# Kernel optimization log

Measured on AMD Instinct MI355X. Metric: run time of the kernel, lower is better.

## Reference

```python
import jax, jax.numpy as jnp
import numpy as np

MAX_LENGTH = 128
SOS_TOKEN = 0

V, H, B, S = 16384, 512, 32, 128


def gru_cell(x, h, Wih, Whh, bih, bhh):
    # torch nn.GRU gate layout: [r, z, n]
    gi = x @ Wih.T + bih  # [B, 3H]
    gh = h @ Whh.T + bhh  # [B, 3H]
    ir, iz, inn = jnp.split(gi, 3, axis=-1)
    hr, hz, hn = jnp.split(gh, 3, axis=-1)
    r = jax.nn.sigmoid(ir + hr)
    z = jax.nn.sigmoid(iz + hz)
    n = jnp.tanh(inn + r * hn)
    return (1.0 - z) * n + z * h


def setup_inputs() -> dict:
    key = jax.random.key(0)
    ks = jax.random.split(key, 13)
    w = lambda k, shape: (jax.random.normal(k, shape, dtype=jnp.float32) * 0.1)
    return {
        "input_tensor": jax.random.randint(ks[0], (B, S), 0, V),
        "enc_emb": w(ks[1], (V, H)),
        "enc_Wih": w(ks[2], (3 * H, H)),
        "enc_Whh": w(ks[3], (3 * H, H)),
        "enc_bih": w(ks[4], (3 * H,)),
        "enc_bhh": w(ks[5], (3 * H,)),
        "dec_emb": w(ks[6], (V, H)),
        "dec_Wih": w(ks[7], (3 * H, H)),
        "dec_Whh": w(ks[8], (3 * H, H)),
        "dec_bih": w(ks[9], (3 * H,)),
        "dec_bhh": w(ks[10], (3 * H,)),
        "out_W": w(ks[11], (V, H)),
        "out_b": w(ks[12], (V,)),
    }


def reference(input_tensor, enc_emb, enc_Wih, enc_Whh, enc_bih, enc_bhh,
              dec_emb, dec_Wih, dec_Whh, dec_bih, dec_bhh, out_W, out_b):
    batch = input_tensor.shape[0]

    # ---- encoder: embedding + GRU over source sequence ----
    xs = enc_emb[input_tensor]                 # [B, S, H]
    xs = jnp.swapaxes(xs, 0, 1)                # [S, B, H]

    def enc_step(h, x):
        h = gru_cell(x, h, enc_Wih, enc_Whh, enc_bih, enc_bhh)
        return h, h

    h0 = jnp.zeros((batch, H), dtype=xs.dtype)
    enc_hidden, enc_outputs = jax.lax.scan(enc_step, h0, xs)
    # enc_outputs: [S, B, H] (unused downstream, as in the original)

    # ---- decoder: free-run (target_tensor=None) with argmax feedback ----
    sos = jnp.full((batch,), SOS_TOKEN, dtype=jnp.int32)

    def dec_step(carry, _):
        h, tok = carry
        x = dec_emb[tok]                       # [B, H]
        h = gru_cell(x, h, dec_Wih, dec_Whh, dec_bih, dec_bhh)
        logits = h @ out_W.T + out_b           # [B, V]
        tok = jnp.argmax(logits, axis=-1).astype(jnp.int32)  # topk(1) feedback
        return (h, tok), logits

    (dec_hidden, _), logits = jax.lax.scan(dec_step, (enc_hidden, sos), None,
                                           length=MAX_LENGTH)
    logits = jnp.swapaxes(logits, 0, 1)        # [B, MAX_LENGTH, V]
    log_probs = jax.nn.log_softmax(logits, axis=-1)
    return log_probs, dec_hidden
```

## Files before the change

kernel.cpp:

```cpp
#include <hip/hip_runtime.h>

#define HDIM 512
#define BATCH 32
#define SEQ 128
#define VOCAB 16384
#define NBLK 256
#define NGRU 128
#define NTHR 256
#define SLOTP 32
#define HLDS_W 516

typedef unsigned long long u64;
typedef unsigned int u32;

static __device__ __forceinline__ u64 aload64(const u64* p) {
    return __hip_atomic_load(p, __ATOMIC_RELAXED, __HIP_MEMORY_SCOPE_AGENT);
}
static __device__ __forceinline__ void astore64(u64* p, u64 v) {
    __hip_atomic_store(p, v, __ATOMIC_RELAXED, __HIP_MEMORY_SCOPE_AGENT);
}
static __device__ __forceinline__ u32 aload32(const u32* p) {
    return __hip_atomic_load(p, __ATOMIC_RELAXED, __HIP_MEMORY_SCOPE_AGENT);
}
static __device__ __forceinline__ void astore32(u32* p, u32 v) {
    __hip_atomic_store(p, v, __ATOMIC_RELAXED, __HIP_MEMORY_SCOPE_AGENT);
}
static __device__ __forceinline__ void astore32f(float* p, float v) {
    __hip_atomic_store((u32*)p, __float_as_uint(v), __ATOMIC_RELAXED,
                       __HIP_MEMORY_SCOPE_AGENT);
}

static __device__ __forceinline__ float4 ld4(const float* p) {
    return *reinterpret_cast<const float4*>(p);
}
static __device__ __forceinline__ float dot4(float4 a, float4 b) {
    return a.x*b.x + a.y*b.y + a.z*b.z + a.w*b.w;
}
static __device__ __forceinline__ u32 ford(float f) {
    u32 b = __float_as_uint(f);
    return b ^ ((b >> 31) ? 0xFFFFFFFFu : 0x80000000u);
}
static __device__ __forceinline__ u64 shfl_xor_u64(u64 x, int m) {
    int lo = __shfl_xor((int)(u32)x, m);
    int hi = __shfl_xor((int)(u32)(x >> 32), m);
    return ((u64)(u32)hi << 32) | (u32)lo;
}

static __device__ __forceinline__ void pollN(const u32* slots, u32 target,
                                             int tid, int per) {
    if (tid < 64) {
        int it = 0;
        for (;;) {
            bool ok = true;
            #pragma unroll
            for (int k = 0; k < 4; ++k)
                if (k < per)
                    ok &= (aload32(&slots[(tid * per + k) * SLOTP]) >= target);
            if (__ballot(ok) == ~0ull) break;
            if (it > 64)      __builtin_amdgcn_s_sleep(16);
            else if (it > 8)  __builtin_amdgcn_s_sleep(2);
            ++it;
        }
    }
    __syncthreads();
    asm volatile("" ::: "memory");
}

static __device__ __forceinline__ void stage_wide(float* hlf, const float* hsrc, int tid) {
    #pragma unroll
    for (int g = 0; g < 2; ++g) {
        float4 v[8];
        #pragma unroll
        for (int k = 0; k < 8; ++k) {
            int q = (g * 8 + k) * NTHR + tid;
            asm volatile("global_load_dwordx4 %0, %1, off sc1"
                         : "=v"(v[k]) : "v"(hsrc + q * 4));
        }
        asm volatile("s_waitcnt vmcnt(0)" ::: "memory");
        __builtin_amdgcn_sched_barrier(0);
        #pragma unroll
        for (int k = 0; k < 8; ++k) {
            int q = (g * 8 + k) * NTHR + tid;
            int w = q * 4;
            *reinterpret_cast<float4*>(hlf + (w >> 9) * HLDS_W + (w & 511)) = v[k];
        }
    }
}

static __device__ __forceinline__ void stage_h(float* hlf, const float* hglob, int tid) {
    const u64* src = (const u64*)hglob;
    #pragma unroll
    for (int it = 0; it < 32; ++it) {
        int q = it * NTHR + tid;
        int w = q * 2;
        u64 v = aload64(src + q);
        *reinterpret_cast<u64*>(hlf + (w >> 9) * HLDS_W + (w & 511)) = v;
    }
}

static __device__ __forceinline__ void gru_core(
    int blk, int tid, const int* toks, const float* hlf, float* hout,
    const float* __restrict__ Wih, const float* __restrict__ Whh,
    const float* __restrict__ bih, const float* __restrict__ bhh,
    const float* __restrict__ emb)
{
    const int wave = tid >> 6;
    const int lane = tid & 63;
    const int kh   = lane >> 5;
    const int b    = lane & 31;
    const int j    = blk * 4 + wave;

    const int tok = toks[b];
    const float* xrow = emb + (size_t)tok * HDIM + kh * 256;
    const float* hrow = hlf + b * HLDS_W + kh * 256;
    const float* wir = Wih + (size_t)(0*HDIM + j) * HDIM + kh * 256;
    const float* wiz = Wih + (size_t)(1*HDIM + j) * HDIM + kh * 256;
    const float* win = Wih + (size_t)(2*HDIM + j) * HDIM + kh * 256;
    const float* whr = Whh + (size_t)(0*HDIM + j) * HDIM + kh * 256;
    const float* whz = Whh + (size_t)(1*HDIM + j) * HDIM + kh * 256;
    const float* whn = Whh + (size_t)(2*HDIM + j) * HDIM + kh * 256;

    float pr = 0.f, pz = 0.f, pxn = 0.f, phn = 0.f;
    #pragma unroll 4
    for (int k4 = 0; k4 < 64; ++k4) {
        float4 x4 = ld4(xrow + k4*4);
        float4 h4 = ld4(hrow + k4*4);
        pr  += dot4(x4, ld4(wir + k4*4)) + dot4(h4, ld4(whr + k4*4));
        pz  += dot4(x4, ld4(wiz + k4*4)) + dot4(h4, ld4(whz + k4*4));
        pxn += dot4(x4, ld4(win + k4*4));
        phn += dot4(h4, ld4(whn + k4*4));
    }
    pr  += __shfl_xor(pr, 32);
    pz  += __shfl_xor(pz, 32);
    pxn += __shfl_xor(pxn, 32);
    phn += __shfl_xor(phn, 32);

    if (kh == 0) {
        float r = 1.f / (1.f + expf(-(pr + bih[j]      + bhh[j])));
        float z = 1.f / (1.f + expf(-(pz + bih[HDIM+j] + bhh[HDIM+j])));
        float n = tanhf(pxn + bih[2*HDIM+j] + r * (phn + bhh[2*HDIM+j]));
        float hprev = hlf[b * HLDS_W + j];
        astore32f(hout + b * HDIM + j, (1.f - z) * n + z * hprev);
    }
}

static __device__ __forceinline__ void logits_core(
    int blk, int tid, const float* hlf,
    const float* __restrict__ outW, const float* __restrict__ outb,
    float* __restrict__ out, int t, u64* pk)
{
    const int vloc = tid & 63;
    const int bq   = tid >> 6;
    const int v    = blk * 64 + vloc;
    const float* wrow = outW + (size_t)v * HDIM;

    float acc[4][8];
    #pragma unroll
    for (int q = 0; q < 4; ++q)
        #pragma unroll
        for (int i = 0; i < 8; ++i) acc[q][i] = 0.f;

    #pragma unroll
    for (int q = 0; q < 4; ++q) {
        for (int k4 = 0; k4 < 32; ++k4) {
            float4 w4 = ld4(wrow + q*128 + k4*4);
            #pragma unroll
            for (int i = 0; i < 8; ++i) {
                float4 h4 = ld4(hlf + (bq*8 + i) * HLDS_W + q*128 + k4*4);
                acc[q][i] += dot4(w4, h4);
            }
        }
    }
    const float vbias = outb[v];
    #pragma unroll
    for (int i = 0; i < 8; ++i) {
        const int b = bq*8 + i;
        float s = ((acc[0][i] + acc[1][i]) + acc[2][i]) + acc[3][i] + vbias;
        __builtin_nontemporal_store(s, &out[(size_t)b*(SEQ*VOCAB) + (size_t)t*VOCAB + v]);
        u64 key = ((u64)ford(s) << 32) | (u32)(~(u32)v);
        #pragma unroll
        for (int d = 1; d < 64; d <<= 1) {
            u64 o = shfl_xor_u64(key, d);
            if (o > key) key = o;
        }
        if (vloc == 0) astore64(pk + b * NBLK + blk, key);
    }
}

static __device__ __forceinline__ void argmax_finalize(
    int tid, const u64* pk, u64 (*redk)[8], int* tok_s)
{
    const int fb = tid >> 3, kc = tid & 7;
    const u64* p = pk + fb * NBLK;
    u64 best = aload64(p + kc);
    #pragma unroll 4
    for (int k = 1; k < 32; ++k) {
        u64 x = aload64(p + kc + k * 8);
        if (x > best) best = x;
    }
    redk[fb][kc] = best;
    __syncthreads();
    if (tid < BATCH) {
        u64 bb = redk[tid][0];
        #pragma unroll
        for (int c = 1; c < 8; ++c) { u64 x = redk[tid][c]; if (x > bb) bb = x; }
        tok_s[tid] = (int)(~(u32)bb);
    }
}

static __device__ __forceinline__ void softmax_row(float* p, int tid,
                                                   float* redm, float* reds) {
    float4 vals[16];
    float m = -3.4e38f;
    #pragma unroll
    for (int i = 0; i < 16; ++i) {
        vals[i] = ld4(p + (i * 256 + tid) * 4);
        m = fmaxf(m, fmaxf(fmaxf(vals[i].x, vals[i].y), fmaxf(vals[i].z, vals[i].w)));
    }
    #pragma unroll
    for (int d = 1; d < 64; d <<= 1) m = fmaxf(m, __shfl_xor(m, d));
    if ((tid & 63) == 0) redm[tid >> 6] = m;
    __syncthreads();
    m = fmaxf(fmaxf(redm[0], redm[1]), fmaxf(redm[2], redm[3]));
    float s = 0.f;
    #pragma unroll
    for (int i = 0; i < 16; ++i) {
        s += expf(vals[i].x - m) + expf(vals[i].y - m)
           + expf(vals[i].z - m) + expf(vals[i].w - m);
    }
    #pragma unroll
    for (int d = 1; d < 64; d <<= 1) s += __shfl_xor(s, d);
    if ((tid & 63) == 0) reds[tid >> 6] = s;
    __syncthreads();
    s = reds[0] + reds[1] + reds[2] + reds[3];
    const float lg = m + logf(s);
    #pragma unroll
    for (int i = 0; i < 16; ++i) {
        float4 r;
        r.x = vals[i].x - lg; r.y = vals[i].y - lg;
        r.z = vals[i].z - lg; r.w = vals[i].w - lg;
        *reinterpret_cast<float4*>(p + (i * 256 + tid) * 4) = r;
    }
    __syncthreads();
}

__global__ __launch_bounds__(NTHR, 1) void seq2seq_main(
    const int* __restrict__ input,
    const float* __restrict__ enc_emb, const float* __restrict__ enc_Wih,
    const float* __restrict__ enc_Whh, const float* __restrict__ enc_bih,
    const float* __restrict__ enc_bhh,
    const float* __restrict__ dec_emb, const float* __restrict__ dec_Wih,
    const float* __restrict__ dec_Whh, const float* __restrict__ dec_bih,
    const float* __restrict__ dec_bhh,
    const float* __restrict__ out_W, const float* __restrict__ out_b,
    float* __restrict__ out, float* hglob, u64* pk,
    u32* hslot, u32* pkslot)
{
    __shared__ __align__(16) float hl[BATCH][HLDS_W];
    __shared__ int tok_s[BATCH];
    __shared__ u64 redk[BATCH][8];

    const int tid = threadIdx.x;
    const int blk = blockIdx.x;
    float* hlf = &hl[0][0];

    for (int i = tid; i < BATCH * HLDS_W; i += NTHR) hlf[i] = 0.f;
    __syncthreads();

    if (blk < NGRU) {
        for (int t = 0; t < SEQ; ++t) {
            float* hgo = hglob + ((t + 1) & 1) * (BATCH * HDIM);
            if (tid < BATCH) tok_s[tid] = input[tid * SEQ + t];
            __syncthreads();
            gru_core(blk, tid, tok_s, hlf, hgo,
                     enc_Wih, enc_Whh, enc_bih, enc_bhh, enc_emb);
            __syncthreads();
            if (tid == 0) astore32(&hslot[blk * SLOTP], (u32)(t + 1));
            pollN(hslot, (u32)(t + 1), tid, 2);
            stage_wide(hlf, hgo, tid);
            __syncthreads();
        }
    }

    for (int t = 0; t < SEQ; ++t) {
        float* hgo = hglob + ((t + 1) & 1) * (BATCH * HDIM);

        if (blk < NGRU) {
            if (t == 0) {
                if (tid < BATCH) tok_s[tid] = 0;
                __syncthreads();
            } else {
                pollN(pkslot, (u32)t, tid, 4);
                argmax_finalize(tid, pk, redk, tok_s);
                __syncthreads();
            }
            gru_core(blk, tid, tok_s, hlf, hgo,
                     dec_Wih, dec_Whh, dec_bih, dec_bhh, dec_emb);
            __syncthreads();
            if (tid == 0) astore32(&hslot[blk * SLOTP], (u32)(SEQ + t + 1));
        }

        pollN(hslot, (u32)(SEQ + t + 1), tid, 2);
        stage_wide(hlf, hgo, tid);
        __syncthreads();
        logits_core(blk, tid, hlf, out_W, out_b, out, t, pk);
        __syncthreads();
        if (tid == 0) astore32(&pkslot[blk * SLOTP], (u32)(t + 1));
    }

    if (blk < 16) {
        const int idx = blk * 1024 + tid * 4;
        const int b = idx >> 9, j = idx & 511;
        *reinterpret_cast<float4*>(out + (size_t)BATCH * SEQ * VOCAB + idx) =
            *reinterpret_cast<const float4*>(&hl[b][j]);
    }
}

#define SLOT_U32 ((128 + 256) * SLOTP)
__global__ __launch_bounds__(256) void init_kernel(float* __restrict__ h0,
                                                   u32* __restrict__ slots) {
    int i = blockIdx.x * 256 + threadIdx.x;
    if (i < BATCH * HDIM) h0[i] = 0.f;
    if (i < SLOT_U32) slots[i] = 0;
}

__global__ __launch_bounds__(256) void gru_step_fb(
    const float* __restrict__ h_in, float* __restrict__ h_out,
    const float* __restrict__ Wih, const float* __restrict__ Whh,
    const float* __restrict__ bih, const float* __restrict__ bhh,
    const float* __restrict__ emb,
    const int* __restrict__ enc_tokens, int t, const u64* __restrict__ pk)
{
    __shared__ __align__(16) float hlt[BATCH][HLDS_W];
    __shared__ int tok_s[BATCH];
    __shared__ u64 redk[BATCH][8];
    const int tid = threadIdx.x;

    if (enc_tokens != nullptr) {
        if (tid < BATCH) tok_s[tid] = enc_tokens[tid * SEQ + t];
    } else if (t == 0) {
        if (tid < BATCH) tok_s[tid] = 0;
    } else {
        argmax_finalize(tid, pk, redk, tok_s);
    }
    stage_h(&hlt[0][0], h_in, tid);
    __syncthreads();
    gru_core(blockIdx.x, tid, tok_s, &hlt[0][0], h_out, Wih, Whh, bih, bhh, emb);
}

__global__ __launch_bounds__(256) void logits_fb(
    const float* __restrict__ h, const float* __restrict__ outW,
    const float* __restrict__ outb, float* __restrict__ out,
    int t, u64* __restrict__ pk)
{
    __shared__ __align__(16) float hlt[BATCH][HLDS_W];
    const int tid = threadIdx.x;
    stage_h(&hlt[0][0], h, tid);
    __syncthreads();
    logits_core(blockIdx.x, tid, &hlt[0][0], outW, outb, out, t, pk);
}

__global__ __launch_bounds__(256) void copy_fb(const float* __restrict__ src,
                                               float* __restrict__ dst, int n) {
    int i = blockIdx.x * 256 + threadIdx.x;
    if (i < n) dst[i] = src[i];
}

__global__ __launch_bounds__(256) void softmax_kernel(float* __restrict__ out) {
    __shared__ float redm[4];
    __shared__ float reds[4];
    softmax_row(out + (size_t)blockIdx.x * VOCAB, threadIdx.x, redm, reds);
}

extern "C" void kernel_launch(void* const* d_in, const int* in_sizes, int n_in,
                              void* d_out, int out_size, void* d_ws, size_t ws_size,
                              hipStream_t stream) {
    const int*   input    = (const int*)  d_in[0];
    const float* enc_emb  = (const float*)d_in[1];
    const float* enc_Wih  = (const float*)d_in[2];
    const float* enc_Whh  = (const float*)d_in[3];
    const float* enc_bih  = (const float*)d_in[4];
    const float* enc_bhh  = (const float*)d_in[5];
    const float* dec_emb  = (const float*)d_in[6];
    const float* dec_Wih  = (const float*)d_in[7];
    const float* dec_Whh  = (const float*)d_in[8];
    const float* dec_bih  = (const float*)d_in[9];
    const float* dec_bhh  = (const float*)d_in[10];
    const float* out_W    = (const float*)d_in[11];
    const float* out_b    = (const float*)d_in[12];

    float* out = (float*)d_out;
    char*  ws  = (char*)d_ws;

    float* hglob  = (float*)ws;
    u64*   pk     = (u64*)(ws + 131072);
    u32*   hslot  = (u32*)(ws + 196608);
    u32*   pkslot = (u32*)(ws + 212992);

    init_kernel<<<dim3(64), dim3(256), 0, stream>>>(hglob, hslot);

    void* args[] = {
        (void*)&input, (void*)&enc_emb, (void*)&enc_Wih, (void*)&enc_Whh,
        (void*)&enc_bih, (void*)&enc_bhh,
        (void*)&dec_emb, (void*)&dec_Wih, (void*)&dec_Whh, (void*)&dec_bih,
        (void*)&dec_bhh, (void*)&out_W, (void*)&out_b,
        (void*)&out, (void*)&hglob, (void*)&pk,
        (void*)&hslot, (void*)&pkslot
    };
    hipError_t rc = hipLaunchCooperativeKernel((void*)seq2seq_main,
                                               dim3(NBLK), dim3(NTHR),
                                               args, 0, stream);
    if (rc != hipSuccess) {
        float* hb[2] = { hglob, hglob + BATCH * HDIM };
        for (int t = 0; t < SEQ; ++t) {
            gru_step_fb<<<dim3(NGRU), dim3(256), 0, stream>>>(
                hb[t & 1], hb[(t + 1) & 1],
                enc_Wih, enc_Whh, enc_bih, enc_bhh, enc_emb, input, t, nullptr);
        }
        for (int t = 0; t < SEQ; ++t) {
            gru_step_fb<<<dim3(NGRU), dim3(256), 0, stream>>>(
                hb[t & 1], hb[(t + 1) & 1],
                dec_Wih, dec_Whh, dec_bih, dec_bhh, dec_emb, nullptr, t, pk);
            logits_fb<<<dim3(NBLK), dim3(256), 0, stream>>>(
                hb[(t + 1) & 1], out_W, out_b, out, t, pk);
        }
        copy_fb<<<dim3((BATCH * HDIM + 255) / 256), dim3(256), 0, stream>>>(
            hglob, out + (size_t)BATCH * SEQ * VOCAB, BATCH * HDIM);
    }

    softmax_kernel<<<dim3(BATCH * SEQ), dim3(256), 0, stream>>>(out);
}
```

Baseline: 9.805 ms.

## Use 1024-thread blocks, fewer GRU blocks, and K-split logits with LDS reduction

Raises the persistent cooperative kernel to 1024 threads per block. GRU rows are now spread over 32 blocks (16 rows each) instead of 128, so fewer blocks take part in each hidden-state barrier poll. The logits GEMV splits the K dimension across four wave groups and reduces partial sums through a new shared-memory buffer before the argmax step. This cuts per-step synchronisation fan-in and adds parallelism to the logits work, at the cost of more LDS, an extra block barrier, and possibly lower occupancy or higher register pressure.

```diff
diff --git a/kernel.cpp b/kernel.cpp
--- a/kernel.cpp
+++ b/kernel.cpp
@@ -5,8 +5,8 @@
 #define SEQ 128
 #define VOCAB 16384
 #define NBLK 256
-#define NGRU 128
-#define NTHR 256
+#define NTHR 1024
+#define NGRU 32
 #define SLOTP 32
 #define HLDS_W 516
 
@@ -47,15 +47,17 @@
 }
 
 static __device__ __forceinline__ void pollN(const u32* slots, u32 target,
-                                             int tid, int per) {
+                                             int tid, int nslots) {
     if (tid < 64) {
+        const int per = (nslots + 63) >> 6;
         int it = 0;
         for (;;) {
             bool ok = true;
-            #pragma unroll
-            for (int k = 0; k < 4; ++k)
-                if (k < per)
-                    ok &= (aload32(&slots[(tid * per + k) * SLOTP]) >= target);
+            for (int k = 0; k < per; ++k) {
+                int idx = tid * per + k;
+                if (idx < nslots)
+                    ok &= (aload32(&slots[idx * SLOTP]) >= target);
+            }
             if (__ballot(ok) == ~0ull) break;
             if (it > 64)      __builtin_amdgcn_s_sleep(16);
             else if (it > 8)  __builtin_amdgcn_s_sleep(2);
@@ -67,23 +69,20 @@
 }
 
 static __device__ __forceinline__ void stage_wide(float* hlf, const float* hsrc, int tid) {
-    #pragma unroll
-    for (int g = 0; g < 2; ++g) {
-        float4 v[8];
-        #pragma unroll
-        for (int k = 0; k < 8; ++k) {
-            int q = (g * 8 + k) * NTHR + tid;
-            asm volatile("global_load_dwordx4 %0, %1, off sc1"
-                         : "=v"(v[k]) : "v"(hsrc + q * 4));
-        }
-        asm volatile("s_waitcnt vmcnt(0)" ::: "memory");
-        __builtin_amdgcn_sched_barrier(0);
-        #pragma unroll
-        for (int k = 0; k < 8; ++k) {
-            int q = (g * 8 + k) * NTHR + tid;
-            int w = q * 4;
-            *reinterpret_cast<float4*>(hlf + (w >> 9) * HLDS_W + (w & 511)) = v[k];
-        }
+    float4 v[4];
+    #pragma unroll
+    for (int k = 0; k < 4; ++k) {
+        int q = k * NTHR + tid;
+        asm volatile("global_load_dwordx4 %0, %1, off sc1"
+                     : "=v"(v[k]) : "v"(hsrc + q * 4));
+    }
+    asm volatile("s_waitcnt vmcnt(0)" ::: "memory");
+    __builtin_amdgcn_sched_barrier(0);
+    #pragma unroll
+    for (int k = 0; k < 4; ++k) {
+        int q = k * NTHR + tid;
+        int w = q * 4;
+        *reinterpret_cast<float4*>(hlf + (w >> 9) * HLDS_W + (w & 511)) = v[k];
     }
 }
 
@@ -91,24 +90,22 @@
     const u64* src = (const u64*)hglob;
     #pragma unroll
     for (int it = 0; it < 32; ++it) {
-        int q = it * NTHR + tid;
+        int q = it * 256 + tid;
         int w = q * 2;
         u64 v = aload64(src + q);
         *reinterpret_cast<u64*>(hlf + (w >> 9) * HLDS_W + (w & 511)) = v;
     }
 }
 
-static __device__ __forceinline__ void gru_core(
-    int blk, int tid, const int* toks, const float* hlf, float* hout,
+static __device__ __forceinline__ void gru_j(
+    int j, int tid, const int* toks, const float* hlf, float* hout,
     const float* __restrict__ Wih, const float* __restrict__ Whh,
     const float* __restrict__ bih, const float* __restrict__ bhh,
     const float* __restrict__ emb)
 {
-    const int wave = tid >> 6;
     const int lane = tid & 63;
     const int kh   = lane >> 5;
     const int b    = lane & 31;
-    const int j    = blk * 4 + wave;
 
     const int tok = toks[b];
     const float* xrow = emb + (size_t)tok * HDIM + kh * 256;
@@ -144,61 +141,20 @@
     }
 }
 
-static __device__ __forceinline__ void logits_core(
-    int blk, int tid, const float* hlf,
-    const float* __restrict__ outW, const float* __restrict__ outb,
-    float* __restrict__ out, int t, u64* pk)
-{
-    const int vloc = tid & 63;
-    const int bq   = tid >> 6;
-    const int v    = blk * 64 + vloc;
-    const float* wrow = outW + (size_t)v * HDIM;
-
-    float acc[4][8];
-    #pragma unroll
-    for (int q = 0; q < 4; ++q)
-        #pragma unroll
-        for (int i = 0; i < 8; ++i) acc[q][i] = 0.f;
-
-    #pragma unroll
-    for (int q = 0; q < 4; ++q) {
-        for (int k4 = 0; k4 < 32; ++k4) {
-            float4 w4 = ld4(wrow + q*128 + k4*4);
-            #pragma unroll
-            for (int i = 0; i < 8; ++i) {
-                float4 h4 = ld4(hlf + (bq*8 + i) * HLDS_W + q*128 + k4*4);
-                acc[q][i] += dot4(w4, h4);
-            }
-        }
-    }
-    const float vbias = outb[v];
-    #pragma unroll
-    for (int i = 0; i < 8; ++i) {
-        const int b = bq*8 + i;
-        float s = ((acc[0][i] + acc[1][i]) + acc[2][i]) + acc[3][i] + vbias;
-        __builtin_nontemporal_store(s, &out[(size_t)b*(SEQ*VOCAB) + (size_t)t*VOCAB + v]);
-        u64 key = ((u64)ford(s) << 32) | (u32)(~(u32)v);
-        #pragma unroll
-        for (int d = 1; d < 64; d <<= 1) {
-            u64 o = shfl_xor_u64(key, d);
-            if (o > key) key = o;
-        }
-        if (vloc == 0) astore64(pk + b * NBLK + blk, key);
-    }
-}
-
-static __device__ __forceinline__ void argmax_finalize(
+static __device__ __forceinline__ void argmax_finalize_w(
     int tid, const u64* pk, u64 (*redk)[8], int* tok_s)
 {
-    const int fb = tid >> 3, kc = tid & 7;
-    const u64* p = pk + fb * NBLK;
-    u64 best = aload64(p + kc);
-    #pragma unroll 4
-    for (int k = 1; k < 32; ++k) {
-        u64 x = aload64(p + kc + k * 8);
-        if (x > best) best = x;
-    }
-    redk[fb][kc] = best;
+    if (tid < 256) {
+        const int fb = tid >> 3, kc = tid & 7;
+        const u64* p = pk + fb * NBLK;
+        u64 best = aload64(p + kc);
+        #pragma unroll 4
+        for (int k = 1; k < 32; ++k) {
+            u64 x = aload64(p + kc + k * 8);
+            if (x > best) best = x;
+        }
+        redk[fb][kc] = best;
+    }
     __syncthreads();
     if (tid < BATCH) {
         u64 bb = redk[tid][0];
@@ -244,7 +200,7 @@
     __syncthreads();
 }
 
-__global__ __launch_bounds__(NTHR, 1) void seq2seq_main(
+__global__ __launch_bounds__(NTHR) void seq2seq_main(
     const int* __restrict__ input,
     const float* __restrict__ enc_emb, const float* __restrict__ enc_Wih,
     const float* __restrict__ enc_Whh, const float* __restrict__ enc_bih,
@@ -257,6 +213,7 @@
     u32* hslot, u32* pkslot)
 {
     __shared__ __align__(16) float hl[BATCH][HLDS_W];
+    __shared__ __align__(16) float part[4][64][33];
     __shared__ int tok_s[BATCH];
     __shared__ u64 redk[BATCH][8];
 
@@ -266,17 +223,20 @@
 
     for (int i = tid; i < BATCH * HLDS_W; i += NTHR) hlf[i] = 0.f;
     __syncthreads();
+
+    const int w = tid >> 6;
+    const int l = tid & 63;
 
     if (blk < NGRU) {
         for (int t = 0; t < SEQ; ++t) {
             float* hgo = hglob + ((t + 1) & 1) * (BATCH * HDIM);
             if (tid < BATCH) tok_s[tid] = input[tid * SEQ + t];
             __syncthreads();
-            gru_core(blk, tid, tok_s, hlf, hgo,
-                     enc_Wih, enc_Whh, enc_bih, enc_bhh, enc_emb);
+            gru_j(blk * 16 + w, tid, tok_s, hlf, hgo,
+                  enc_Wih, enc_Whh, enc_bih, enc_bhh, enc_emb);
             __syncthreads();
             if (tid == 0) astore32(&hslot[blk * SLOTP], (u32)(t + 1));
-            pollN(hslot, (u32)(t + 1), tid, 2);
+            pollN(hslot, (u32)(t + 1), tid, NGRU);
             stage_wide(hlf, hgo, tid);
             __syncthreads();
         }
@@ -290,38 +250,103 @@
                 if (tid < BATCH) tok_s[tid] = 0;
                 __syncthreads();
             } else {
-                pollN(pkslot, (u32)t, tid, 4);
-                argmax_finalize(tid, pk, redk, tok_s);
+                pollN(pkslot, (u32)t, tid, NBLK);
+                argmax_finalize_w(tid, pk, redk, tok_s);
                 __syncthreads();
             }
-            gru_core(blk, tid, tok_s, hlf, hgo,
-                     dec_Wih, dec_Whh, dec_bih, dec_bhh, dec_emb);
+            gru_j(blk * 16 + w, tid, tok_s, hlf, hgo,
+                  dec_Wih, dec_Whh, dec_bih, dec_bhh, dec_emb);
             __syncthreads();
             if (tid == 0) astore32(&hslot[blk * SLOTP], (u32)(SEQ + t + 1));
         }
 
-        pollN(hslot, (u32)(SEQ + t + 1), tid, 2);
+        pollN(hslot, (u32)(SEQ + t + 1), tid, NGRU);
         stage_wide(hlf, hgo, tid);
         __syncthreads();
-        logits_core(blk, tid, hlf, out_W, out_b, out, t, pk);
+
+        {
+            const int ks = w & 3;
+            const int vq = w >> 2;
+            const int vloc = vq * 16 + (l >> 2);
+            const int bg = l & 3;
+            const int v = blk * 64 + vloc;
+            const float* wrow = out_W + (size_t)v * HDIM + ks * 128;
+
+            float acc[8];
+            #pragma unroll
+            for (int i = 0; i < 8; ++i) acc[i] = 0.f;
+            for (int k4 = 0; k4 < 32; ++k4) {
+                float4 w4 = ld4(wrow + k4*4);
+                #pragma unroll
+                for (int i = 0; i < 8; ++i) {
+                    float4 h4 = ld4(hlf + (bg*8 + i) * HLDS_W + ks*128 + k4*4);
+                    acc[i] += dot4(w4, h4);
+                }
+            }
+            #pragma unroll
+            for (int i = 0; i < 8; ++i) part[ks][vloc][bg*8 + i] = acc[i];
+        }
+        __syncthreads();
+
+        {
+            const int v = blk * 64 + l;
+            const float vbias = out_b[v];
+            #pragma unroll
+            for (int i = 0; i < 2; ++i) {
+                const int b = w * 2 + i;
+                float s = ((part[0][l][b] + part[1][l][b]) + part[2][l][b])
+                          + part[3][l][b] + vbias;
+                __builtin_nontemporal_store(s,
+                    &out[(size_t)b*(SEQ*VOCAB) + (size_t)t*VOCAB + v]);
+                u64 key = ((u64)ford(s) << 32) | (u32)(~(u32)v);
+                #pragma unroll
+                for (int d = 1; d < 64; d <<= 1) {
+                    u64 o = shfl_xor_u64(key, d);
+                    if (o > key) key = o;
+                }
+                if (l == 0) astore64(&pk[b * NBLK + blk], key);
+            }
+        }
         __syncthreads();
         if (tid == 0) astore32(&pkslot[blk * SLOTP], (u32)(t + 1));
     }
 
-    if (blk < 16) {
-        const int idx = blk * 1024 + tid * 4;
+    if (blk < 4) {
+        const int idx = blk * 4096 + tid * 4;
         const int b = idx >> 9, j = idx & 511;
         *reinterpret_cast<float4*>(out + (size_t)BATCH * SEQ * VOCAB + idx) =
             *reinterpret_cast<const float4*>(&hl[b][j]);
     }
 }
 
-#define SLOT_U32 ((128 + 256) * SLOTP)
 __global__ __launch_bounds__(256) void init_kernel(float* __restrict__ h0,
-                                                   u32* __restrict__ slots) {
+                                                   u32* __restrict__ hslot,
+                                                   u32* __restrict__ pkslot) {
     int i = blockIdx.x * 256 + threadIdx.x;
     if (i < BATCH * HDIM) h0[i] = 0.f;
-    if (i < SLOT_U32) slots[i] = 0;
+    if (i < NGRU * SLOTP) hslot[i] = 0;
+    if (i < NBLK * SLOTP) pkslot[i] = 0;
+}
+
+static __device__ __forceinline__ void argmax_finalize(
+    int tid, const u64* pk, u64 (*redk)[8], int* tok_s)
+{
+    const int fb = tid >> 3, kc = tid & 7;
+    const u64* p = pk + fb * NBLK;
+    u64 best = aload64(p + kc);
+    #pragma unroll 4
+    for (int k = 1; k < 32; ++k) {
+        u64 x = aload64(p + kc + k * 8);
+        if (x > best) best = x;
+    }
+    redk[fb][kc] = best;
+    __syncthreads();
+    if (tid < BATCH) {
+        u64 bb = redk[tid][0];
+        #pragma unroll
+        for (int c = 1; c < 8; ++c) { u64 x = redk[tid][c]; if (x > bb) bb = x; }
+        tok_s[tid] = (int)(~(u32)bb);
+    }
 }
 
 __global__ __launch_bounds__(256) void gru_step_fb(
@@ -345,7 +370,8 @@
     }
     stage_h(&hlt[0][0], h_in, tid);
     __syncthreads();
-    gru_core(blockIdx.x, tid, tok_s, &hlt[0][0], h_out, Wih, Whh, bih, bhh, emb);
+    gru_j(blockIdx.x * 4 + (tid >> 6), tid, tok_s, &hlt[0][0], h_out,
+          Wih, Whh, bih, bhh, emb);
 }
 
 __global__ __launch_bounds__(256) void logits_fb(
@@ -357,7 +383,40 @@
     const int tid = threadIdx.x;
     stage_h(&hlt[0][0], h, tid);
     __syncthreads();
-    logits_core(blockIdx.x, tid, &hlt[0][0], outW, outb, out, t, pk);
+
+    const int vloc = tid & 63;
+    const int bq   = tid >> 6;
+    const int v    = blockIdx.x * 64 + vloc;
+    const float* wrow = outW + (size_t)v * HDIM;
+    const float* hlf = &hlt[0][0];
+
+    float acc[4][8];
+    #pragma unroll
+    for (int q = 0; q < 4; ++q)
+        #pragma unroll
+        for (int i = 0; i < 8; ++i) acc[q][i] = 0.f;
+    #pragma unroll
+    for (int q = 0; q < 4; ++q)
+        for (int k4 = 0; k4 < 32; ++k4) {
+            float4 w4 = ld4(wrow + q*128 + k4*4);
+            #pragma unroll
+            for (int i = 0; i < 8; ++i)
+                acc[q][i] += dot4(w4, ld4(hlf + (bq*8 + i) * HLDS_W + q*128 + k4*4));
+        }
+    const float vbias = outb[v];
+    #pragma unroll
+    for (int i = 0; i < 8; ++i) {
+        const int b = bq*8 + i;
+        float s = ((acc[0][i] + acc[1][i]) + acc[2][i]) + acc[3][i] + vbias;
+        out[(size_t)b * (SEQ * VOCAB) + (size_t)t * VOCAB + v] = s;
+        u64 key = ((u64)ford(s) << 32) | (u32)(~(u32)v);
+        #pragma unroll
+        for (int d = 1; d < 64; d <<= 1) {
+            u64 o = shfl_xor_u64(key, d);
+            if (o > key) key = o;
+        }
+        if (vloc == 0) astore64(pk + b * NBLK + blockIdx.x, key);
+    }
 }
 
 __global__ __launch_bounds__(256) void copy_fb(const float* __restrict__ src,
@@ -395,9 +454,9 @@
     float* hglob  = (float*)ws;
     u64*   pk     = (u64*)(ws + 131072);
     u32*   hslot  = (u32*)(ws + 196608);
-    u32*   pkslot = (u32*)(ws + 212992);
-
-    init_kernel<<<dim3(64), dim3(256), 0, stream>>>(hglob, hslot);
+    u32*   pkslot = (u32*)(ws + 200704);
+
+    init_kernel<<<dim3(64), dim3(256), 0, stream>>>(hglob, hslot, pkslot);
 
     void* args[] = {
         (void*)&input, (void*)&enc_emb, (void*)&enc_Wih, (void*)&enc_Whh,
@@ -413,12 +472,12 @@
     if (rc != hipSuccess) {
         float* hb[2] = { hglob, hglob + BATCH * HDIM };
         for (int t = 0; t < SEQ; ++t) {
-            gru_step_fb<<<dim3(NGRU), dim3(256), 0, stream>>>(
+            gru_step_fb<<<dim3(128), dim3(256), 0, stream>>>(
                 hb[t & 1], hb[(t + 1) & 1],
                 enc_Wih, enc_Whh, enc_bih, enc_bhh, enc_emb, input, t, nullptr);
         }
         for (int t = 0; t < SEQ; ++t) {
-            gru_step_fb<<<dim3(NGRU), dim3(256), 0, stream>>>(
+            gru_step_fb<<<dim3(128), dim3(256), 0, stream>>>(
                 hb[t & 1], hb[(t + 1) & 1],
                 dec_Wih, dec_Whh, dec_bih, dec_bhh, dec_emb, nullptr, t, pk);
             logits_fb<<<dim3(NBLK), dim3(256), 0, stream>>>(
```

New measurement: 25.16 ms. 157% more time.

## Replace all-to-all slot polling with aggregator blocks and distributed argmax tokens

Applied to the files above, without the earlier changes.

Instead of every block polling all 128 GRU slots or all 256 logit slots, designated blocks (255 for hidden state, 254 for logits) gather completion and publish a single go flag that other blocks poll with one thread. The argmax finalize is split so that each of 32 blocks reduces one batch row and publishes its token with a step tag, which GRU blocks then gather. This is meant to cut global polling traffic and the redundant full argmax reduction on every block, at the cost of an extra hop of latency through the aggregator and extra load on blocks 254 and 255.

```diff
diff --git a/kernel.cpp b/kernel.cpp
--- a/kernel.cpp
+++ b/kernel.cpp
@@ -12,6 +12,7 @@
 
 typedef unsigned long long u64;
 typedef unsigned int u32;
+typedef __attribute__((ext_vector_type(2))) unsigned long long u64x2;
 
 static __device__ __forceinline__ u64 aload64(const u64* p) {
     return __hip_atomic_load(p, __ATOMIC_RELAXED, __HIP_MEMORY_SCOPE_AGENT);
@@ -47,16 +48,31 @@
 }
 
 static __device__ __forceinline__ void pollN(const u32* slots, u32 target,
-                                             int tid, int per) {
+                                             int tid, int nslots) {
     if (tid < 64) {
+        const int per = (nslots + 63) >> 6;
         int it = 0;
         for (;;) {
             bool ok = true;
-            #pragma unroll
-            for (int k = 0; k < 4; ++k)
-                if (k < per)
-                    ok &= (aload32(&slots[(tid * per + k) * SLOTP]) >= target);
+            for (int k = 0; k < per; ++k) {
+                int idx = tid * per + k;
+                if (idx < nslots)
+                    ok &= (aload32(&slots[idx * SLOTP]) >= target);
+            }
             if (__ballot(ok) == ~0ull) break;
+            if (it > 64)      __builtin_amdgcn_s_sleep(16);
+            else if (it > 8)  __builtin_amdgcn_s_sleep(2);
+            ++it;
+        }
+    }
+    __syncthreads();
+    asm volatile("" ::: "memory");
+}
+
+static __device__ __forceinline__ void poll1(const u32* line, u32 target, int tid) {
+    if (tid == 0) {
+        int it = 0;
+        while (aload32(line) < target) {
             if (it > 64)      __builtin_amdgcn_s_sleep(16);
             else if (it > 8)  __builtin_amdgcn_s_sleep(2);
             ++it;
@@ -91,24 +107,22 @@
     const u64* src = (const u64*)hglob;
     #pragma unroll
     for (int it = 0; it < 32; ++it) {
-        int q = it * NTHR + tid;
+        int q = it * 256 + tid;
         int w = q * 2;
         u64 v = aload64(src + q);
         *reinterpret_cast<u64*>(hlf + (w >> 9) * HLDS_W + (w & 511)) = v;
     }
 }
 
-static __device__ __forceinline__ void gru_core(
-    int blk, int tid, const int* toks, const float* hlf, float* hout,
+static __device__ __forceinline__ void gru_j(
+    int j, int tid, const int* toks, const float* hlf, float* hout,
     const float* __restrict__ Wih, const float* __restrict__ Whh,
     const float* __restrict__ bih, const float* __restrict__ bhh,
     const float* __restrict__ emb)
 {
-    const int wave = tid >> 6;
     const int lane = tid & 63;
     const int kh   = lane >> 5;
     const int b    = lane & 31;
-    const int j    = blk * 4 + wave;
 
     const int tok = toks[b];
     const float* xrow = emb + (size_t)tok * HDIM + kh * 256;
@@ -254,11 +268,10 @@
     const float* __restrict__ dec_bhh,
     const float* __restrict__ out_W, const float* __restrict__ out_b,
     float* __restrict__ out, float* hglob, u64* pk,
-    u32* hslot, u32* pkslot)
+    u32* hslot, u32* pkslot, u32* go_h, u32* go_pk, u64* tokline)
 {
     __shared__ __align__(16) float hl[BATCH][HLDS_W];
     __shared__ int tok_s[BATCH];
-    __shared__ u64 redk[BATCH][8];
 
     const int tid = threadIdx.x;
     const int blk = blockIdx.x;
@@ -266,19 +279,26 @@
 
     for (int i = tid; i < BATCH * HLDS_W; i += NTHR) hlf[i] = 0.f;
     __syncthreads();
+
+    const int w = tid >> 6;
 
     if (blk < NGRU) {
         for (int t = 0; t < SEQ; ++t) {
             float* hgo = hglob + ((t + 1) & 1) * (BATCH * HDIM);
             if (tid < BATCH) tok_s[tid] = input[tid * SEQ + t];
             __syncthreads();
-            gru_core(blk, tid, tok_s, hlf, hgo,
-                     enc_Wih, enc_Whh, enc_bih, enc_bhh, enc_emb);
+            gru_j(blk * 4 + w, tid, tok_s, hlf, hgo,
+                  enc_Wih, enc_Whh, enc_bih, enc_bhh, enc_emb);
             __syncthreads();
             if (tid == 0) astore32(&hslot[blk * SLOTP], (u32)(t + 1));
-            pollN(hslot, (u32)(t + 1), tid, 2);
+            poll1(go_h, (u32)(t + 1), tid);
             stage_wide(hlf, hgo, tid);
             __syncthreads();
+        }
+    } else if (blk == 255) {
+        for (int t = 0; t < SEQ; ++t) {
+            pollN(hslot, (u32)(t + 1), tid, NGRU);
+            if (tid == 0) astore32(go_h, (u32)(t + 1));
         }
     }
 
@@ -290,22 +310,68 @@
                 if (tid < BATCH) tok_s[tid] = 0;
                 __syncthreads();
             } else {
-                pollN(pkslot, (u32)t, tid, 4);
-                argmax_finalize(tid, pk, redk, tok_s);
+                if (blk < BATCH) {
+                    poll1(go_pk, (u32)t, tid);
+                    if (tid < 64) {
+                        const u64* prow = pk + (size_t)blk * NBLK + tid * 4;
+                        u64x2 a, b2;
+                        asm volatile("global_load_dwordx4 %0, %1, off sc1"
+                                     : "=v"(a) : "v"(prow));
+                        asm volatile("global_load_dwordx4 %0, %1, off sc1"
+                                     : "=v"(b2) : "v"(prow + 2));
+                        asm volatile("s_waitcnt vmcnt(0)" ::: "memory");
+                        u64 best = a.x;
+                        if (a.y  > best) best = a.y;
+                        if (b2.x > best) best = b2.x;
+                        if (b2.y > best) best = b2.y;
+                        #pragma unroll
+                        for (int d = 1; d < 64; d <<= 1) {
+                            u64 o = shfl_xor_u64(best, d);
+                            if (o > best) best = o;
+                        }
+                        if (tid == 0)
+                            astore64(&tokline[blk * 16],
+                                     ((u64)(u32)t << 32) | (u32)(~(u32)best));
+                    }
+                }
+                if (tid < 64) {
+                    u64 tv = 0; int it = 0;
+                    for (;;) {
+                        bool ok = true;
+                        if (tid < 32) {
+                            tv = aload64(&tokline[tid * 16]);
+                            ok = ((u32)(tv >> 32) >= (u32)t);
+                        }
+                        if (__ballot(ok) == ~0ull) break;
+                        if (it > 64)      __builtin_amdgcn_s_sleep(16);
+                        else if (it > 8)  __builtin_amdgcn_s_sleep(2);
+                        ++it;
+                    }
+                    if (tid < 32) tok_s[tid] = (int)(u32)tv;
+                }
                 __syncthreads();
             }
-            gru_core(blk, tid, tok_s, hlf, hgo,
-                     dec_Wih, dec_Whh, dec_bih, dec_bhh, dec_emb);
+            gru_j(blk * 4 + w, tid, tok_s, hlf, hgo,
+                  dec_Wih, dec_Whh, dec_bih, dec_bhh, dec_emb);
             __syncthreads();
             if (tid == 0) astore32(&hslot[blk * SLOTP], (u32)(SEQ + t + 1));
         }
 
-        pollN(hslot, (u32)(SEQ + t + 1), tid, 2);
+        if (blk == 255) {
+            pollN(hslot, (u32)(SEQ + t + 1), tid, NGRU);
+            if (tid == 0) astore32(go_h, (u32)(SEQ + t + 1));
+        } else {
+            poll1(go_h, (u32)(SEQ + t + 1), tid);
+        }
         stage_wide(hlf, hgo, tid);
         __syncthreads();
         logits_core(blk, tid, hlf, out_W, out_b, out, t, pk);
         __syncthreads();
         if (tid == 0) astore32(&pkslot[blk * SLOTP], (u32)(t + 1));
+        if (blk == 254) {
+            pollN(pkslot, (u32)(t + 1), tid, NBLK);
+            if (tid == 0) astore32(go_pk, (u32)(t + 1));
+        }
     }
 
     if (blk < 16) {
@@ -316,12 +382,15 @@
     }
 }
 
-#define SLOT_U32 ((128 + 256) * SLOTP)
 __global__ __launch_bounds__(256) void init_kernel(float* __restrict__ h0,
-                                                   u32* __restrict__ slots) {
+                                                   u32* __restrict__ hslot,
+                                                   u32* __restrict__ pkslot,
+                                                   u32* __restrict__ extra) {
     int i = blockIdx.x * 256 + threadIdx.x;
     if (i < BATCH * HDIM) h0[i] = 0.f;
-    if (i < SLOT_U32) slots[i] = 0;
+    if (i < NGRU * SLOTP) hslot[i] = 0;
+    if (i < NBLK * SLOTP) pkslot[i] = 0;
+    if (i < 1088) extra[i] = 0;
 }
 
 __global__ __launch_bounds__(256) void gru_step_fb(
@@ -345,7 +414,8 @@
     }
     stage_h(&hlt[0][0], h_in, tid);
     __syncthreads();
-    gru_core(blockIdx.x, tid, tok_s, &hlt[0][0], h_out, Wih, Whh, bih, bhh, emb);
+    gru_j(blockIdx.x * 4 + (tid >> 6), tid, tok_s, &hlt[0][0], h_out,
+          Wih, Whh, bih, bhh, emb);
 }
 
 __global__ __launch_bounds__(256) void logits_fb(
@@ -392,12 +462,16 @@
     float* out = (float*)d_out;
     char*  ws  = (char*)d_ws;
 
-    float* hglob  = (float*)ws;
-    u64*   pk     = (u64*)(ws + 131072);
-    u32*   hslot  = (u32*)(ws + 196608);
-    u32*   pkslot = (u32*)(ws + 212992);
-
-    init_kernel<<<dim3(64), dim3(256), 0, stream>>>(hglob, hslot);
+    float* hglob   = (float*)ws;
+    u64*   pk      = (u64*)(ws + 131072);
+    u32*   hslot   = (u32*)(ws + 196608);
+    u32*   pkslot  = (u32*)(ws + 212992);
+    u32*   extra   = (u32*)(ws + 245760);
+    u32*   go_h    = extra;
+    u32*   go_pk   = extra + SLOTP;
+    u64*   tokline = (u64*)(extra + 2 * SLOTP);
+
+    init_kernel<<<dim3(64), dim3(256), 0, stream>>>(hglob, hslot, pkslot, extra);
 
     void* args[] = {
         (void*)&input, (void*)&enc_emb, (void*)&enc_Wih, (void*)&enc_Whh,
@@ -405,7 +479,7 @@
         (void*)&dec_emb, (void*)&dec_Wih, (void*)&dec_Whh, (void*)&dec_bih,
         (void*)&dec_bhh, (void*)&out_W, (void*)&out_b,
         (void*)&out, (void*)&hglob, (void*)&pk,
-        (void*)&hslot, (void*)&pkslot
+        (void*)&hslot, (void*)&pkslot, (void*)&go_h, (void*)&go_pk, (void*)&tokline
     };
     hipError_t rc = hipLaunchCooperativeKernel((void*)seq2seq_main,
                                                dim3(NBLK), dim3(NTHR),
@@ -413,12 +487,12 @@
     if (rc != hipSuccess) {
         float* hb[2] = { hglob, hglob + BATCH * HDIM };
         for (int t = 0; t < SEQ; ++t) {
-            gru_step_fb<<<dim3(NGRU), dim3(256), 0, stream>>>(
+            gru_step_fb<<<dim3(128), dim3(256), 0, stream>>>(
                 hb[t & 1], hb[(t + 1) & 1],
                 enc_Wih, enc_Whh, enc_bih, enc_bhh, enc_emb, input, t, nullptr);
         }
         for (int t = 0; t < SEQ; ++t) {
-            gru_step_fb<<<dim3(NGRU), dim3(256), 0, stream>>>(
+            gru_step_fb<<<dim3(128), dim3(256), 0, stream>>>(
                 hb[t & 1], hb[(t + 1) & 1],
                 dec_Wih, dec_Whh, dec_bih, dec_bhh, dec_emb, nullptr, t, pk);
             logits_fb<<<dim3(NBLK), dim3(256), 0, stream>>>(
```

Result: slower. 10.17 ms (+3.7%).
